# Kernel tuning notes

Measured on AMD Instinct MI355X. Metric: run time of the kernel, lower is better.

The kernel has to match this reference:

```python
import jax, jax.numpy as jnp
import numpy as np

K = 9            # box-filter size per axis
PAD = (K - 1) // 2
KSIZE = K * K * K  # 729


def _box_sum(x):
    """Separable 9x9x9 box sum with zero padding (same math as conv3d with all-ones kernel)."""
    for i in range(3):  # loop over the 3 spatial axes (fixed small structural loop)
        ks = [1, 1, 1]
        ks[i] = K
        pad = [(0, 0)] * 3
        pad[i] = (PAD, PAD)
        kern = jnp.ones((1, 1, *ks), x.dtype)
        x = jax.lax.conv_general_dilated(
            x, kern, window_strides=(1, 1, 1), padding=pad,
            dimension_numbers=('NCDHW', 'OIDHW', 'NCDHW'))
    return x


def setup_inputs() -> dict:
    key = jax.random.key(0)
    k1, k2 = jax.random.split(key)
    shape = (2, 1, 160, 192, 160)
    return {
        'input': jax.random.normal(k1, shape, dtype=jnp.float32),
        'target': jax.random.normal(k2, shape, dtype=jnp.float32),
    }


def reference(input, target):
    # target rescaled from (-1, 1) to (0, 1), as in the torch module
    target = (target + 1.0) * 0.5

    II = input * input
    TT = target * target
    IT = input * target

    T_sum = _box_sum(target)
    I_sum = _box_sum(input)
    TT_sum = _box_sum(TT)
    II_sum = _box_sum(II)
    IT_sum = _box_sum(IT)

    Ihat = I_sum / KSIZE
    That = T_sum / KSIZE

    cross = IT_sum - Ihat * T_sum - That * I_sum + That * Ihat * KSIZE
    T_var = TT_sum - 2.0 * That * T_sum + That * That * KSIZE
    I_var = II_sum - 2.0 * Ihat * I_sum + Ihat * Ihat * KSIZE

    cc = cross * cross / (T_var * I_var + 1e-5)
    return -1.0 * jnp.mean(cc)
```

## Files before the change

### kernel.cpp

```cpp
#include <hip/hip_runtime.h>

namespace {

typedef _Float16 half_t;
typedef _Float16 half2_t __attribute__((ext_vector_type(2)));
typedef _Float16 half4_t __attribute__((ext_vector_type(4)));
typedef _Float16 half8_t __attribute__((ext_vector_type(8)));

constexpr int Wd = 160, Hd = 192, Dd = 160;
constexpr int TX = 16, TY = 16, CZ = 80;
constexpr int HW = Hd * Wd;
constexpr int LIVE = CZ + 8;
constexpr float INV_K = 1.0f / 729.0f;
constexpr float INV_TOT = 1.0f / 9830400.0f;
constexpr int R8 = 17;
constexpr int ROWS = 24;


__global__ __launch_bounds__(256)
void ncc_main(const float* __restrict__ inp, const float* __restrict__ tgt,
              float* __restrict__ out)
{
    __shared__ half8_t xs8[2][ROWS * R8];
    __shared__ half4_t ringAB[9 * 256];
    __shared__ half_t  ringT[9 * 256];
    __shared__ float   red[4];

    const int tid = threadIdx.x;

    const int lin = (int)blockIdx.x + 10 * (int)blockIdx.y + 120 * (int)blockIdx.z;
    const int swz = (lin & 7) * 60 + (lin >> 3);
    const int bx = swz % 10;
    const int by = (swz / 10) % 12;
    const int bz = swz / 120;

    const int n  = bz >> 1;
    const int zc = bz & 1;
    const int x0 = bx * TX, y0 = by * TY, z0 = zc * CZ;

    #pragma unroll
    for (int q = 0; q < 9; ++q) {
        ringAB[q * 256 + tid] = (half4_t)0;
        ringT[q * 256 + tid] = (half_t)0.f;
    }

    const bool isProd = (tid >= 128) && (tid < 224);
    const int up = (tid >= 128) ? (tid - 128) : 0;
    const int r  = (up < 96) ? (up >> 2) : 0;
    const int hq = up & 3;
    const int h  = hq >> 1, qx = hq & 1;
    const int gy = y0 - 4 + r;
    const bool yok = (gy >= 0) && (gy < Hd);
    const int gyc = min(max(gy, 0), Hd - 1);
    const int gxs = x0 - 4 + 8 * h + 4 * qx;

#define DECODE(c) \
    int voff##c; float m##c; \
    { const int gx = gxs + 4 * (c); \
      m##c = (yok && gx >= 0 && gx < Wd) ? 1.f : 0.f; \
      const int gxc = min(max(gx, 0), Wd - 4); \
      voff##c = gyc * Wd + gxc; }
    DECODE(0) DECODE(1) DECODE(2)
#undef DECODE

    const int nb = n * (Dd * HW);
    const float* baseI = inp + nb;
    const float* baseT = tgt + nb;

    const int col0 = 8 * h + 4 * qx;
    half_t* const sb0 = (half_t*)xs8[0] + (r * R8 + col0) * 8;
    half_t* const sb1 = (half_t*)xs8[1] + (r * R8 + col0) * 8;

    const int xi = tid & 15;
    const int yp = (tid >> 4) & 7;
    const bool p2on = tid < 128;
    const half8_t* const rd8_0 = &xs8[0][(2 * yp) * R8 + xi];
    const half8_t* const rd8_1 = &xs8[1][(2 * yp) * R8 + xi];

    float4 S4a = make_float4(0.f, 0.f, 0.f, 0.f);
    float4 S4b = make_float4(0.f, 0.f, 0.f, 0.f);
    float STa = 0.f, STb = 0.f, acc = 0.f;

    float4 SI0, SI1, SI2, ST0, ST1, ST2;
    SI0 = SI1 = SI2 = ST0 = ST1 = ST2 = make_float4(0.f, 0.f, 0.f, 0.f);

#define PRELOAD(zz) { \
    const float* pI = baseI + (zz) * HW; \
    const float* pT = baseT + (zz) * HW; \
    SI0 = *(const float4*)(pI + voff0); ST0 = *(const float4*)(pT + voff0); \
    SI1 = *(const float4*)(pI + voff1); ST1 = *(const float4*)(pT + voff1); \
    SI2 = *(const float4*)(pI + voff2); ST2 = *(const float4*)(pT + voff2); }

#define F4E(v, e) ((e) == 0 ? (v).x : ((e) == 1 ? (v).y : ((e) == 2 ? (v).z : (v).w)))

#define WIN4(PP, W) { \
    float ss = PP[0] + PP[1] + PP[2] + PP[3] + PP[4] + PP[5] + PP[6] + PP[7] + PP[8]; \
    W[0] = ss; ss += PP[9]  - PP[0]; W[1] = ss; \
               ss += PP[10] - PP[1]; W[2] = ss; \
               ss += PP[11] - PP[2]; W[3] = ss; }

#define PRODUCE(SBP) { \
    float Im[12], Tr[12], p[12]; \
    float wII[4], wIT[4], wTT[4], wI[4], wT[4]; \
    _Pragma("unroll") \
    for (int e = 0; e < 4; ++e) { \
        Im[e]     = F4E(SI0, e) * m0;  Tr[e]     = fmaf(F4E(ST0, e), 0.5f, 0.5f); \
        Im[4 + e] = F4E(SI1, e) * m1;  Tr[4 + e] = fmaf(F4E(ST1, e), 0.5f, 0.5f); \
        Im[8 + e] = F4E(SI2, e) * m2;  Tr[8 + e] = fmaf(F4E(ST2, e), 0.5f, 0.5f); } \
    _Pragma("unroll") \
    for (int i = 0; i < 12; ++i) \
        p[i] = Im[i] * F4E((i < 4 ? SI0 : (i < 8 ? SI1 : SI2)), i & 3); \
    WIN4(p, wII) \
    _Pragma("unroll") \
    for (int i = 0; i < 12; ++i) p[i] = Im[i] * Tr[i]; \
    WIN4(p, wIT) \
    WIN4(Im, wI) \
    _Pragma("unroll") \
    for (int i = 0; i < 12; ++i) Im[i] = Tr[i] * (i < 4 ? m0 : (i < 8 ? m1 : m2)); \
    _Pragma("unroll") \
    for (int i = 0; i < 12; ++i) p[i] = Im[i] * Tr[i]; \
    WIN4(p, wTT) \
    WIN4(Im, wT) \
    _Pragma("unroll") \
    for (int cc = 0; cc < 4; ++cc) { \
        const half2_t v01 = {(half_t)wII[cc], (half_t)wIT[cc]}; \
        const half2_t v23 = {(half_t)wTT[cc], (half_t)wI[cc]}; \
        ((half2_t*)(SBP))[cc * 4]     = v01; \
        ((half2_t*)(SBP))[cc * 4 + 1] = v23; \
        (SBP)[cc * 8 + 4] = (half_t)wT[cc]; } }

    if (isProd) {
        if (z0 - 4 >= 0) { PRELOAD(z0 - 4) PRODUCE(sb0) }
        if (z0 - 3 >= 0) PRELOAD(z0 - 3)
    }
    __syncthreads();

#define STEP_BODY(UU) { \
    const int k = tb + (UU); \
    if (isProd) { \
        const int zi1 = z0 - 3 + k;              \
        if ((k + 1) < LIVE && zi1 >= 0 && zi1 < Dd) { \
            if (((UU) & 1) == 0) PRODUCE(sb1) else PRODUCE(sb0) \
        } \
        const int zi2 = z0 - 2 + k;              \
        if ((k + 2) < LIVE && zi2 >= 0 && zi2 < Dd) PRELOAD(zi2) \
    } \
    {  \
        const int zi = z0 - 4 + k; \
        const bool zok = (zi >= 0) && (zi < Dd); \
        half2_t a01_0 = (half2_t)0, a23_0 = (half2_t)0; \
        half2_t a01_1 = (half2_t)0, a23_1 = (half2_t)0; \
        half_t aT0 = (half_t)0.f, aT1 = (half_t)0.f; \
        if (zok && p2on) { \
            const half8_t* const rd8 = (((UU) & 1) != 0) ? rd8_1 : rd8_0; \
            const half8_t w0 = rd8[0]; \
            const half8_t w9 = rd8[9 * R8]; \
            half2_t m01 = (half2_t)0, m23 = (half2_t)0, m4 = (half2_t)0; \
            _Pragma("unroll") \
            for (int kk = 1; kk < 9; ++kk) { \
                const half8_t w = rd8[kk * R8]; \
                const half2_t* wp = (const half2_t*)&w; \
                m01 += wp[0]; m23 += wp[1]; m4 += wp[2]; \
            } \
            const half2_t* w0p = (const half2_t*)&w0; \
            const half2_t* w9p = (const half2_t*)&w9; \
            a01_0 = m01 + w0p[0]; a23_0 = m23 + w0p[1]; aT0 = m4.x + w0p[2].x; \
            a01_1 = m01 + w9p[0]; a23_1 = m23 + w9p[1]; aT1 = m4.x + w9p[2].x; \
        } \
        if (p2on) { \
            const int sl = (UU) % 9;             \
            half8_t* const rAB8 = (half8_t*)&ringAB[sl * 256 + 2 * tid]; \
            half2_t* const rT  = (half2_t*)&ringT[sl * 256 + 2 * tid]; \
            const half8_t oA = *rAB8; \
            const half2_t oT = *rT; \
            S4a.x += (float)a01_0.x - (float)oA[0]; \
            S4a.y += (float)a01_0.y - (float)oA[1]; \
            S4a.z += (float)a23_0.x - (float)oA[2]; \
            S4a.w += (float)a23_0.y - (float)oA[3]; \
            STa   += (float)aT0 - (float)oT.x; \
            S4b.x += (float)a01_1.x - (float)oA[4]; \
            S4b.y += (float)a01_1.y - (float)oA[5]; \
            S4b.z += (float)a23_1.x - (float)oA[6]; \
            S4b.w += (float)a23_1.y - (float)oA[7]; \
            STb   += (float)aT1 - (float)oT.y; \
            const half8_t nA = {a01_0.x, a01_0.y, a23_0.x, a23_0.y, \
                                a01_1.x, a01_1.y, a23_1.x, a23_1.y}; \
            *rAB8 = nA; \
            const half2_t nT = {aT0, aT1}; \
            *rT = nT; \
        } \
        if (k >= 8 && p2on) {                    \
            { const float sii = S4a.x, sit = S4a.y, stt = S4a.z, si = S4a.w, stv = STa; \
              const float cross = sit - si * stv * INV_K; \
              const float tvar  = stt - stv * stv * INV_K; \
              const float ivar  = sii - si  * si  * INV_K; \
              acc += cross * cross * __builtin_amdgcn_rcpf(tvar * ivar + 1e-5f); } \
            { const float sii = S4b.x, sit = S4b.y, stt = S4b.z, si = S4b.w, stv = STb; \
              const float cross = sit - si * stv * INV_K; \
              const float tvar  = stt - stv * stv * INV_K; \
              const float ivar  = sii - si  * si  * INV_K; \
              acc += cross * cross * __builtin_amdgcn_rcpf(tvar * ivar + 1e-5f); } \
        } \
    } \
    __syncthreads(); }

    for (int tb = 0; tb < 90; tb += 18) {
        #pragma unroll
        for (int uu = 0; uu < 18; ++uu) {
            if (tb + uu < LIVE) STEP_BODY(uu)
        }
    }
#undef STEP_BODY
#undef PRODUCE
#undef WIN4
#undef F4E
#undef PRELOAD

    #pragma unroll
    for (int off = 32; off > 0; off >>= 1) acc += __shfl_down(acc, off, 64);
    if ((tid & 63) == 0) red[tid >> 6] = acc;
    __syncthreads();
    if (tid == 0) {
        const float tot = red[0] + red[1] + red[2] + red[3];
        atomicAdd(out, -tot * INV_TOT);
    }
}

}

extern "C" void kernel_launch(void* const* d_in, const int* in_sizes, int n_in,
                              void* d_out, int out_size, void* d_ws, size_t ws_size,
                              hipStream_t stream)
{
    const float* inp = (const float*)d_in[0];
    const float* tgt = (const float*)d_in[1];
    float* out = (float*)d_out;

    hipMemsetAsync(d_out, 0, sizeof(float), stream);
    dim3 grid(Wd / TX, Hd / TY, 2 * (Dd / CZ));
    ncc_main<<<grid, 256, 0, stream>>>(inp, tgt, out);
}
```

Before: 152.2 us.

## Process two z-slices per barrier with quad-buffered shared staging

Restructures the producer/consumer z-loop so each iteration produces two slices and consumes two slices between a single __syncthreads, halving the number of block barriers. Shared staging grows from two to four half8 buffers, and two register sets of prefetched input/target rows are kept live. The cost being removed is barrier overhead and serialization between the producer and consumer halves. The extra register set and doubled staging LDS may reduce occupancy or raise register pressure.

```diff
diff --git a/kernel.cpp b/kernel.cpp
--- a/kernel.cpp
+++ b/kernel.cpp
@@ -11,6 +11,7 @@
 constexpr int TX = 16, TY = 16, CZ = 80;
 constexpr int HW = Hd * Wd;
 constexpr int LIVE = CZ + 8;
+constexpr int NSTEP = LIVE / 2;
 constexpr float INV_K = 1.0f / 729.0f;
 constexpr float INV_TOT = 1.0f / 9830400.0f;
 constexpr int R8 = 17;
@@ -21,7 +22,7 @@
 void ncc_main(const float* __restrict__ inp, const float* __restrict__ tgt,
               float* __restrict__ out)
 {
-    __shared__ half8_t xs8[2][ROWS * R8];
+    __shared__ half8_t xs8[4][ROWS * R8];
     __shared__ half4_t ringAB[9 * 256];
     __shared__ half_t  ringT[9 * 256];
     __shared__ float   red[4];
@@ -70,26 +71,33 @@
     const int col0 = 8 * h + 4 * qx;
     half_t* const sb0 = (half_t*)xs8[0] + (r * R8 + col0) * 8;
     half_t* const sb1 = (half_t*)xs8[1] + (r * R8 + col0) * 8;
+    half_t* const sb2 = (half_t*)xs8[2] + (r * R8 + col0) * 8;
+    half_t* const sb3 = (half_t*)xs8[3] + (r * R8 + col0) * 8;
 
     const int xi = tid & 15;
     const int yp = (tid >> 4) & 7;
     const bool p2on = tid < 128;
     const half8_t* const rd8_0 = &xs8[0][(2 * yp) * R8 + xi];
     const half8_t* const rd8_1 = &xs8[1][(2 * yp) * R8 + xi];
+    const half8_t* const rd8_2 = &xs8[2][(2 * yp) * R8 + xi];
+    const half8_t* const rd8_3 = &xs8[3][(2 * yp) * R8 + xi];
 
     float4 S4a = make_float4(0.f, 0.f, 0.f, 0.f);
     float4 S4b = make_float4(0.f, 0.f, 0.f, 0.f);
     float STa = 0.f, STb = 0.f, acc = 0.f;
 
-    float4 SI0, SI1, SI2, ST0, ST1, ST2;
-    SI0 = SI1 = SI2 = ST0 = ST1 = ST2 = make_float4(0.f, 0.f, 0.f, 0.f);
-
-#define PRELOAD(zz) { \
+#define DECL_SET(S) \
+    float4 SI0##S, SI1##S, SI2##S, ST0##S, ST1##S, ST2##S; \
+    SI0##S = SI1##S = SI2##S = ST0##S = ST1##S = ST2##S = make_float4(0.f, 0.f, 0.f, 0.f);
+    DECL_SET(A) DECL_SET(B)
+#undef DECL_SET
+
+#define PRELOAD(S, zz) { \
     const float* pI = baseI + (zz) * HW; \
     const float* pT = baseT + (zz) * HW; \
-    SI0 = *(const float4*)(pI + voff0); ST0 = *(const float4*)(pT + voff0); \
-    SI1 = *(const float4*)(pI + voff1); ST1 = *(const float4*)(pT + voff1); \
-    SI2 = *(const float4*)(pI + voff2); ST2 = *(const float4*)(pT + voff2); }
+    SI0##S = *(const float4*)(pI + voff0); ST0##S = *(const float4*)(pT + voff0); \
+    SI1##S = *(const float4*)(pI + voff1); ST1##S = *(const float4*)(pT + voff1); \
+    SI2##S = *(const float4*)(pI + voff2); ST2##S = *(const float4*)(pT + voff2); }
 
 #define F4E(v, e) ((e) == 0 ? (v).x : ((e) == 1 ? (v).y : ((e) == 2 ? (v).z : (v).w)))
 
@@ -99,17 +107,17 @@
                ss += PP[10] - PP[1]; W[2] = ss; \
                ss += PP[11] - PP[2]; W[3] = ss; }
 
-#define PRODUCE(SBP) { \
+#define PRODUCE(S, SBP) { \
     float Im[12], Tr[12], p[12]; \
     float wII[4], wIT[4], wTT[4], wI[4], wT[4]; \
     _Pragma("unroll") \
     for (int e = 0; e < 4; ++e) { \
-        Im[e]     = F4E(SI0, e) * m0;  Tr[e]     = fmaf(F4E(ST0, e), 0.5f, 0.5f); \
-        Im[4 + e] = F4E(SI1, e) * m1;  Tr[4 + e] = fmaf(F4E(ST1, e), 0.5f, 0.5f); \
-        Im[8 + e] = F4E(SI2, e) * m2;  Tr[8 + e] = fmaf(F4E(ST2, e), 0.5f, 0.5f); } \
+        Im[e]     = F4E(SI0##S, e) * m0;  Tr[e]     = fmaf(F4E(ST0##S, e), 0.5f, 0.5f); \
+        Im[4 + e] = F4E(SI1##S, e) * m1;  Tr[4 + e] = fmaf(F4E(ST1##S, e), 0.5f, 0.5f); \
+        Im[8 + e] = F4E(SI2##S, e) * m2;  Tr[8 + e] = fmaf(F4E(ST2##S, e), 0.5f, 0.5f); } \
     _Pragma("unroll") \
     for (int i = 0; i < 12; ++i) \
-        p[i] = Im[i] * F4E((i < 4 ? SI0 : (i < 8 ? SI1 : SI2)), i & 3); \
+        p[i] = Im[i] * F4E((i < 4 ? SI0##S : (i < 8 ? SI1##S : SI2##S)), i & 3); \
     WIN4(p, wII) \
     _Pragma("unroll") \
     for (int i = 0; i < 12; ++i) p[i] = Im[i] * Tr[i]; \
@@ -129,88 +137,101 @@
         ((half2_t*)(SBP))[cc * 4 + 1] = v23; \
         (SBP)[cc * 8 + 4] = (half_t)wT[cc]; } }
 
+#define CONSUME(S, RD8, SLOT) { \
+    const int zi = z0 - 4 + (S); \
+    const bool zok = (zi >= 0) && (zi < Dd); \
+    half2_t a01_0 = (half2_t)0, a23_0 = (half2_t)0; \
+    half2_t a01_1 = (half2_t)0, a23_1 = (half2_t)0; \
+    half_t aT0 = (half_t)0.f, aT1 = (half_t)0.f; \
+    if (zok && p2on) { \
+        const half8_t w0 = (RD8)[0]; \
+        const half8_t w9 = (RD8)[9 * R8]; \
+        half2_t m01 = (half2_t)0, m23 = (half2_t)0, m4 = (half2_t)0; \
+        _Pragma("unroll") \
+        for (int kk = 1; kk < 9; ++kk) { \
+            const half8_t w = (RD8)[kk * R8]; \
+            const half2_t* wp = (const half2_t*)&w; \
+            m01 += wp[0]; m23 += wp[1]; m4 += wp[2]; \
+        } \
+        const half2_t* w0p = (const half2_t*)&w0; \
+        const half2_t* w9p = (const half2_t*)&w9; \
+        a01_0 = m01 + w0p[0]; a23_0 = m23 + w0p[1]; aT0 = m4.x + w0p[2].x; \
+        a01_1 = m01 + w9p[0]; a23_1 = m23 + w9p[1]; aT1 = m4.x + w9p[2].x; \
+    } \
+    if (p2on) {  \
+        half8_t* const rAB8 = (half8_t*)&ringAB[(SLOT) * 256 + 2 * tid]; \
+        half2_t* const rT  = (half2_t*)&ringT[(SLOT) * 256 + 2 * tid]; \
+        const half8_t oA = *rAB8; \
+        const half2_t oT = *rT; \
+        S4a.x += (float)a01_0.x - (float)oA[0]; \
+        S4a.y += (float)a01_0.y - (float)oA[1]; \
+        S4a.z += (float)a23_0.x - (float)oA[2]; \
+        S4a.w += (float)a23_0.y - (float)oA[3]; \
+        STa   += (float)aT0 - (float)oT.x; \
+        S4b.x += (float)a01_1.x - (float)oA[4]; \
+        S4b.y += (float)a01_1.y - (float)oA[5]; \
+        S4b.z += (float)a23_1.x - (float)oA[6]; \
+        S4b.w += (float)a23_1.y - (float)oA[7]; \
+        STb   += (float)aT1 - (float)oT.y; \
+        const half8_t nA = {a01_0.x, a01_0.y, a23_0.x, a23_0.y, \
+                            a01_1.x, a01_1.y, a23_1.x, a23_1.y}; \
+        *rAB8 = nA; \
+        const half2_t nT = {aT0, aT1}; \
+        *rT = nT; \
+    } \
+    if ((S) >= 8 && p2on) {                    \
+        { const float sii = S4a.x, sit = S4a.y, stt = S4a.z, si = S4a.w, stv = STa; \
+          const float cross = sit - si * stv * INV_K; \
+          const float tvar  = stt - stv * stv * INV_K; \
+          const float ivar  = sii - si  * si  * INV_K; \
+          acc += cross * cross * __builtin_amdgcn_rcpf(tvar * ivar + 1e-5f); } \
+        { const float sii = S4b.x, sit = S4b.y, stt = S4b.z, si = S4b.w, stv = STb; \
+          const float cross = sit - si * stv * INV_K; \
+          const float tvar  = stt - stv * stv * INV_K; \
+          const float ivar  = sii - si  * si  * INV_K; \
+          acc += cross * cross * __builtin_amdgcn_rcpf(tvar * ivar + 1e-5f); } \
+    } }
+
     if (isProd) {
-        if (z0 - 4 >= 0) { PRELOAD(z0 - 4) PRODUCE(sb0) }
-        if (z0 - 3 >= 0) PRELOAD(z0 - 3)
+        if (z0 - 4 >= 0) { PRELOAD(A, z0 - 4) PRODUCE(A, sb0) }
+        if (z0 - 3 >= 0) { PRELOAD(B, z0 - 3) PRODUCE(B, sb1) }
+        if (z0 - 2 >= 0) PRELOAD(A, z0 - 2)
+        if (z0 - 1 >= 0) PRELOAD(B, z0 - 1)
     }
     __syncthreads();
 
-#define STEP_BODY(UU) { \
-    const int k = tb + (UU); \
+#define STEP_BODY(JJ, SL0, SL1, CB0, CB1, PB0, PB1) { \
+    const int j = jb + (JJ); \
+    const int s0 = 2 * j; \
     if (isProd) { \
-        const int zi1 = z0 - 3 + k;              \
-        if ((k + 1) < LIVE && zi1 >= 0 && zi1 < Dd) { \
-            if (((UU) & 1) == 0) PRODUCE(sb1) else PRODUCE(sb0) \
-        } \
-        const int zi2 = z0 - 2 + k;              \
-        if ((k + 2) < LIVE && zi2 >= 0 && zi2 < Dd) PRELOAD(zi2) \
+        const int za = z0 - 2 + s0;              \
+        if ((s0 + 2) < LIVE && za >= 0 && za < Dd) PRODUCE(A, sb##PB0) \
+        const int zb = za + 1;                   \
+        if ((s0 + 3) < LIVE && zb >= 0 && zb < Dd) PRODUCE(B, sb##PB1) \
+        if ((s0 + 4) < LIVE && (za + 2) < Dd) PRELOAD(A, za + 2) \
+        if ((s0 + 5) < LIVE && (zb + 2) < Dd) PRELOAD(B, zb + 2) \
     } \
-    {  \
-        const int zi = z0 - 4 + k; \
-        const bool zok = (zi >= 0) && (zi < Dd); \
-        half2_t a01_0 = (half2_t)0, a23_0 = (half2_t)0; \
-        half2_t a01_1 = (half2_t)0, a23_1 = (half2_t)0; \
-        half_t aT0 = (half_t)0.f, aT1 = (half_t)0.f; \
-        if (zok && p2on) { \
-            const half8_t* const rd8 = (((UU) & 1) != 0) ? rd8_1 : rd8_0; \
-            const half8_t w0 = rd8[0]; \
-            const half8_t w9 = rd8[9 * R8]; \
-            half2_t m01 = (half2_t)0, m23 = (half2_t)0, m4 = (half2_t)0; \
-            _Pragma("unroll") \
-            for (int kk = 1; kk < 9; ++kk) { \
-                const half8_t w = rd8[kk * R8]; \
-                const half2_t* wp = (const half2_t*)&w; \
-                m01 += wp[0]; m23 += wp[1]; m4 += wp[2]; \
-            } \
-            const half2_t* w0p = (const half2_t*)&w0; \
-            const half2_t* w9p = (const half2_t*)&w9; \
-            a01_0 = m01 + w0p[0]; a23_0 = m23 + w0p[1]; aT0 = m4.x + w0p[2].x; \
-            a01_1 = m01 + w9p[0]; a23_1 = m23 + w9p[1]; aT1 = m4.x + w9p[2].x; \
-        } \
-        if (p2on) { \
-            const int sl = (UU) % 9;             \
-            half8_t* const rAB8 = (half8_t*)&ringAB[sl * 256 + 2 * tid]; \
-            half2_t* const rT  = (half2_t*)&ringT[sl * 256 + 2 * tid]; \
-            const half8_t oA = *rAB8; \
-            const half2_t oT = *rT; \
-            S4a.x += (float)a01_0.x - (float)oA[0]; \
-            S4a.y += (float)a01_0.y - (float)oA[1]; \
-            S4a.z += (float)a23_0.x - (float)oA[2]; \
-            S4a.w += (float)a23_0.y - (float)oA[3]; \
-            STa   += (float)aT0 - (float)oT.x; \
-            S4b.x += (float)a01_1.x - (float)oA[4]; \
-            S4b.y += (float)a01_1.y - (float)oA[5]; \
-            S4b.z += (float)a23_1.x - (float)oA[6]; \
-            S4b.w += (float)a23_1.y - (float)oA[7]; \
-            STb   += (float)aT1 - (float)oT.y; \
-            const half8_t nA = {a01_0.x, a01_0.y, a23_0.x, a23_0.y, \
-                                a01_1.x, a01_1.y, a23_1.x, a23_1.y}; \
-            *rAB8 = nA; \
-            const half2_t nT = {aT0, aT1}; \
-            *rT = nT; \
-        } \
-        if (k >= 8 && p2on) {                    \
-            { const float sii = S4a.x, sit = S4a.y, stt = S4a.z, si = S4a.w, stv = STa; \
-              const float cross = sit - si * stv * INV_K; \
-              const float tvar  = stt - stv * stv * INV_K; \
-              const float ivar  = sii - si  * si  * INV_K; \
-              acc += cross * cross * __builtin_amdgcn_rcpf(tvar * ivar + 1e-5f); } \
-            { const float sii = S4b.x, sit = S4b.y, stt = S4b.z, si = S4b.w, stv = STb; \
-              const float cross = sit - si * stv * INV_K; \
-              const float tvar  = stt - stv * stv * INV_K; \
-              const float ivar  = sii - si  * si  * INV_K; \
-              acc += cross * cross * __builtin_amdgcn_rcpf(tvar * ivar + 1e-5f); } \
-        } \
-    } \
+    CONSUME(s0,     rd8_##CB0, SL0) \
+    CONSUME(s0 + 1, rd8_##CB1, SL1) \
     __syncthreads(); }
 
-    for (int tb = 0; tb < 90; tb += 18) {
-        #pragma unroll
-        for (int uu = 0; uu < 18; ++uu) {
-            if (tb + uu < LIVE) STEP_BODY(uu)
-        }
-    }
+#define STEP(JJ, SL0, SL1, CB0, CB1, PB0, PB1) \
+    if (jb + (JJ) < NSTEP) STEP_BODY(JJ, SL0, SL1, CB0, CB1, PB0, PB1)
+
+    for (int jb = 0; jb < 54; jb += 18) {
+        STEP(0,  0, 1, 0, 1, 2, 3)  STEP(1,  2, 3, 2, 3, 0, 1)
+        STEP(2,  4, 5, 0, 1, 2, 3)  STEP(3,  6, 7, 2, 3, 0, 1)
+        STEP(4,  8, 0, 0, 1, 2, 3)  STEP(5,  1, 2, 2, 3, 0, 1)
+        STEP(6,  3, 4, 0, 1, 2, 3)  STEP(7,  5, 6, 2, 3, 0, 1)
+        STEP(8,  7, 8, 0, 1, 2, 3)  STEP(9,  0, 1, 2, 3, 0, 1)
+        STEP(10, 2, 3, 0, 1, 2, 3)  STEP(11, 4, 5, 2, 3, 0, 1)
+        STEP(12, 6, 7, 0, 1, 2, 3)  STEP(13, 8, 0, 2, 3, 0, 1)
+        STEP(14, 1, 2, 0, 1, 2, 3)  STEP(15, 3, 4, 2, 3, 0, 1)
+        STEP(16, 5, 6, 0, 1, 2, 3)  STEP(17, 7, 8, 2, 3, 0, 1)
+    }
+#undef STEP
 #undef STEP_BODY
+#undef CONSUME
 #undef PRODUCE
 #undef WIN4
 #undef F4E
```

Result: slower. 156.1 us (+2.5%).

## Software-pipeline the Y-window consumer by one step to hide LDS latency

Applied to the files above, without the earlier changes.

The consumer stage now issues the shared-memory loads for the current Y-window and the ring-buffer slot first. It then applies the Z-ring update and the NCC accumulation using the window sums computed in the previous step, and only afterwards reduces the freshly loaded rows into sums for the next step. The ring slot indices are shifted by one, with an epilogue step after the loop. The aim is to overlap LDS read latency with the arithmetic. The cost is extra live registers (ten half8 values plus the carried sums) and more complex ring indexing.

```diff
diff --git a/kernel.cpp b/kernel.cpp
--- a/kernel.cpp
+++ b/kernel.cpp
@@ -81,6 +81,10 @@
     float4 S4b = make_float4(0.f, 0.f, 0.f, 0.f);
     float STa = 0.f, STb = 0.f, acc = 0.f;
 
+    half2_t pa01_0 = (half2_t)0, pa23_0 = (half2_t)0;
+    half2_t pa01_1 = (half2_t)0, pa23_1 = (half2_t)0;
+    half2_t paT = (half2_t)0;
+
     float4 SI0, SI1, SI2, ST0, ST1, ST2;
     SI0 = SI1 = SI2 = ST0 = ST1 = ST2 = make_float4(0.f, 0.f, 0.f, 0.f);
 
@@ -135,7 +139,7 @@
     }
     __syncthreads();
 
-#define STEP_BODY(UU) { \
+#define STEP_BODY(UU, SLP) { \
     const int k = tb + (UU); \
     if (isProd) { \
         const int zi1 = z0 - 3 + k;              \
@@ -145,51 +149,37 @@
         const int zi2 = z0 - 2 + k;              \
         if ((k + 2) < LIVE && zi2 >= 0 && zi2 < Dd) PRELOAD(zi2) \
     } \
-    {  \
+    { \
         const int zi = z0 - 4 + k; \
         const bool zok = (zi >= 0) && (zi < Dd); \
-        half2_t a01_0 = (half2_t)0, a23_0 = (half2_t)0; \
-        half2_t a01_1 = (half2_t)0, a23_1 = (half2_t)0; \
-        half_t aT0 = (half_t)0.f, aT1 = (half_t)0.f; \
-        if (zok && p2on) { \
+        const bool rdok = zok && p2on; \
+        half8_t oA = (half8_t)0; half2_t oT = (half2_t)0; \
+        half8_t* const rAB8 = (half8_t*)&ringAB[(SLP) * 256 + 2 * tid]; \
+        half2_t* const rT  = (half2_t*)&ringT[(SLP) * 256 + 2 * tid]; \
+        if (p2on) { oA = *rAB8; oT = *rT; }      \
+        half8_t w[10]; \
+        if (rdok) {                              \
             const half8_t* const rd8 = (((UU) & 1) != 0) ? rd8_1 : rd8_0; \
-            const half8_t w0 = rd8[0]; \
-            const half8_t w9 = rd8[9 * R8]; \
-            half2_t m01 = (half2_t)0, m23 = (half2_t)0, m4 = (half2_t)0; \
             _Pragma("unroll") \
-            for (int kk = 1; kk < 9; ++kk) { \
-                const half8_t w = rd8[kk * R8]; \
-                const half2_t* wp = (const half2_t*)&w; \
-                m01 += wp[0]; m23 += wp[1]; m4 += wp[2]; \
-            } \
-            const half2_t* w0p = (const half2_t*)&w0; \
-            const half2_t* w9p = (const half2_t*)&w9; \
-            a01_0 = m01 + w0p[0]; a23_0 = m23 + w0p[1]; aT0 = m4.x + w0p[2].x; \
-            a01_1 = m01 + w9p[0]; a23_1 = m23 + w9p[1]; aT1 = m4.x + w9p[2].x; \
-        } \
-        if (p2on) { \
-            const int sl = (UU) % 9;             \
-            half8_t* const rAB8 = (half8_t*)&ringAB[sl * 256 + 2 * tid]; \
-            half2_t* const rT  = (half2_t*)&ringT[sl * 256 + 2 * tid]; \
-            const half8_t oA = *rAB8; \
-            const half2_t oT = *rT; \
-            S4a.x += (float)a01_0.x - (float)oA[0]; \
-            S4a.y += (float)a01_0.y - (float)oA[1]; \
-            S4a.z += (float)a23_0.x - (float)oA[2]; \
-            S4a.w += (float)a23_0.y - (float)oA[3]; \
-            STa   += (float)aT0 - (float)oT.x; \
-            S4b.x += (float)a01_1.x - (float)oA[4]; \
-            S4b.y += (float)a01_1.y - (float)oA[5]; \
-            S4b.z += (float)a23_1.x - (float)oA[6]; \
-            S4b.w += (float)a23_1.y - (float)oA[7]; \
-            STb   += (float)aT1 - (float)oT.y; \
-            const half8_t nA = {a01_0.x, a01_0.y, a23_0.x, a23_0.y, \
-                                a01_1.x, a01_1.y, a23_1.x, a23_1.y}; \
+            for (int kk = 0; kk < 10; ++kk) w[kk] = rd8[kk * R8]; \
+        } \
+        if (p2on) {                              \
+            S4a.x += (float)pa01_0.x - (float)oA[0]; \
+            S4a.y += (float)pa01_0.y - (float)oA[1]; \
+            S4a.z += (float)pa23_0.x - (float)oA[2]; \
+            S4a.w += (float)pa23_0.y - (float)oA[3]; \
+            STa   += (float)paT.x - (float)oT.x; \
+            S4b.x += (float)pa01_1.x - (float)oA[4]; \
+            S4b.y += (float)pa01_1.y - (float)oA[5]; \
+            S4b.z += (float)pa23_1.x - (float)oA[6]; \
+            S4b.w += (float)pa23_1.y - (float)oA[7]; \
+            STb   += (float)paT.y - (float)oT.y; \
+            const half8_t nA = {pa01_0.x, pa01_0.y, pa23_0.x, pa23_0.y, \
+                                pa01_1.x, pa01_1.y, pa23_1.x, pa23_1.y}; \
             *rAB8 = nA; \
-            const half2_t nT = {aT0, aT1}; \
-            *rT = nT; \
-        } \
-        if (k >= 8 && p2on) {                    \
+            *rT = paT; \
+        } \
+        if (k >= 9 && p2on) {                    \
             { const float sii = S4a.x, sit = S4a.y, stt = S4a.z, si = S4a.w, stv = STa; \
               const float cross = sit - si * stv * INV_K; \
               const float tvar  = stt - stv * stv * INV_K; \
@@ -201,16 +191,64 @@
               const float ivar  = sii - si  * si  * INV_K; \
               acc += cross * cross * __builtin_amdgcn_rcpf(tvar * ivar + 1e-5f); } \
         } \
+        if (rdok) {                              \
+            half2_t m01 = (half2_t)0, m23 = (half2_t)0, m4 = (half2_t)0; \
+            _Pragma("unroll") \
+            for (int kk = 1; kk < 9; ++kk) { \
+                const half2_t* wp = (const half2_t*)&w[kk]; \
+                m01 += wp[0]; m23 += wp[1]; m4 += wp[2]; \
+            } \
+            const half2_t* w0p = (const half2_t*)&w[0]; \
+            const half2_t* w9p = (const half2_t*)&w[9]; \
+            pa01_0 = m01 + w0p[0]; pa23_0 = m23 + w0p[1]; \
+            pa01_1 = m01 + w9p[0]; pa23_1 = m23 + w9p[1]; \
+            const half2_t nT = {m4.x + w0p[2].x, m4.x + w9p[2].x}; \
+            paT = nT; \
+        } else { \
+            pa01_0 = (half2_t)0; pa23_0 = (half2_t)0; \
+            pa01_1 = (half2_t)0; pa23_1 = (half2_t)0; \
+            paT = (half2_t)0; \
+        } \
     } \
     __syncthreads(); }
 
+#define STEP(UU, SLP) if (tb + (UU) < LIVE) STEP_BODY(UU, SLP)
+
     for (int tb = 0; tb < 90; tb += 18) {
-        #pragma unroll
-        for (int uu = 0; uu < 18; ++uu) {
-            if (tb + uu < LIVE) STEP_BODY(uu)
-        }
-    }
+        STEP(0, 8)  STEP(1, 0)  STEP(2, 1)  STEP(3, 2)  STEP(4, 3)
+        STEP(5, 4)  STEP(6, 5)  STEP(7, 6)  STEP(8, 7)  STEP(9, 8)
+        STEP(10, 0) STEP(11, 1) STEP(12, 2) STEP(13, 3) STEP(14, 4)
+        STEP(15, 5) STEP(16, 6) STEP(17, 7)
+    }
+#undef STEP
 #undef STEP_BODY
+
+    if (p2on) {
+        half8_t* const rAB8 = (half8_t*)&ringAB[6 * 256 + 2 * tid];
+        half2_t* const rT  = (half2_t*)&ringT[6 * 256 + 2 * tid];
+        const half8_t oA = *rAB8;
+        const half2_t oT = *rT;
+        S4a.x += (float)pa01_0.x - (float)oA[0];
+        S4a.y += (float)pa01_0.y - (float)oA[1];
+        S4a.z += (float)pa23_0.x - (float)oA[2];
+        S4a.w += (float)pa23_0.y - (float)oA[3];
+        STa   += (float)paT.x - (float)oT.x;
+        S4b.x += (float)pa01_1.x - (float)oA[4];
+        S4b.y += (float)pa01_1.y - (float)oA[5];
+        S4b.z += (float)pa23_1.x - (float)oA[6];
+        S4b.w += (float)pa23_1.y - (float)oA[7];
+        STb   += (float)paT.y - (float)oT.y;
+        { const float sii = S4a.x, sit = S4a.y, stt = S4a.z, si = S4a.w, stv = STa;
+          const float cross = sit - si * stv * INV_K;
+          const float tvar  = stt - stv * stv * INV_K;
+          const float ivar  = sii - si  * si  * INV_K;
+          acc += cross * cross * __builtin_amdgcn_rcpf(tvar * ivar + 1e-5f); }
+        { const float sii = S4b.x, sit = S4b.y, stt = S4b.z, si = S4b.w, stv = STb;
+          const float cross = sit - si * stv * INV_K;
+          const float tvar  = stt - stv * stv * INV_K;
+          const float ivar  = sii - si  * si  * INV_K;
+          acc += cross * cross * __builtin_amdgcn_rcpf(tvar * ivar + 1e-5f); }
+    }
 #undef PRODUCE
 #undef WIN4
 #undef F4E
```

Measured after the change: 415.1 us. 173% more time.
